# Performance work log

Measured on AMD Instinct MI355X. Metric: run time of the kernel, lower is better.

## Reference

```python
import jax, jax.numpy as jnp
import numpy as np

N, T, F_IN, F_OUT, E = 20000, 4, 64, 64, 640000


def setup_inputs() -> dict:
    key = jax.random.key(0)
    k1, k2, k3, k4, k5, k6 = jax.random.split(key, 6)
    node_features = jax.random.normal(k1, (N, T, F_IN), dtype=jnp.float32)
    edge_weights = jax.random.uniform(k2, (T, E), dtype=jnp.float32)
    src = jax.random.randint(k3, (E,), 0, N, dtype=jnp.int32)
    dst = jax.random.randint(k4, (E,), 0, N, dtype=jnp.int32)
    W = jax.random.normal(k5, (F_OUT, F_IN), dtype=jnp.float32) / np.sqrt(F_IN)
    b = jax.random.normal(k6, (F_OUT,), dtype=jnp.float32) * 0.01
    return {"node_features": node_features, "edge_weights": edge_weights,
            "src": src, "dst": dst, "W": W, "b": b}


def reference(node_features, edge_weights, src, dst, W, b):
    # u_mul_e: gather source node features and scale by per-edge, per-time weight
    # edge_weights (T, E) -> transposed (E, T) -> broadcast over feature dim
    msg = node_features[src] * edge_weights.T[:, :, None]          # (E, T, F_IN)
    # fn.sum: scatter-sum messages into destination nodes
    h = jax.ops.segment_sum(msg, dst, num_segments=node_features.shape[0])  # (N, T, F_IN)
    # nn.Linear(in_features, out_features)
    return h @ W.T + b                                             # (N, T, F_OUT)
```

## Files before the change

### kernel.cpp

```cpp
#include <hip/hip_runtime.h>

#define N_NODES 20000
#define T_STEPS 4
#define F_DIM   64
#define E_EDGES 640000
#define ROWS    (N_NODES * T_STEPS)
#define ROW_ELEMS (T_STEPS * F_DIM)

#define SCATTER_BLOCKS   (E_EDGES / 1024)
#define TRANSFORM_BLOCKS (ROWS / 64)
#define OVF_CAP          4096

__device__ __forceinline__ unsigned short f32_to_bf16_rne(float f) {
    unsigned u = __float_as_uint(f);
    u += 0x7FFFu + ((u >> 16) & 1u);
    return (unsigned short)(u >> 16);
}
__device__ __forceinline__ float bf16_to_f32(unsigned short h) {
    return __uint_as_float((unsigned)h << 16);
}

__global__ __launch_bounds__(256) void fused_build_kernel(
    const float* __restrict__ x, const float* __restrict__ W,
    unsigned short* __restrict__ yb,
    const int* __restrict__ src, const int* __restrict__ dst,
    const float* __restrict__ ew,
    int* __restrict__ cnt, int4* __restrict__ buckets, int cap,
    int4* __restrict__ ovf, int* __restrict__ ovf_cnt)
{
    if (blockIdx.x < SCATTER_BLOCKS) {
        const int base = blockIdx.x * 1024 + threadIdx.x;
#pragma unroll
        for (int j = 0; j < 4; ++j) {
            const int e = base + j * 256;
            const int d = dst[e];
            int4 rec;
            rec.x = src[e];
            rec.y = (unsigned)f32_to_bf16_rne(ew[e]) |
                    ((unsigned)f32_to_bf16_rne(ew[E_EDGES + e]) << 16);
            rec.z = (unsigned)f32_to_bf16_rne(ew[2 * E_EDGES + e]) |
                    ((unsigned)f32_to_bf16_rne(ew[3 * E_EDGES + e]) << 16);
            rec.w = d;
            const int pos = atomicAdd(&cnt[d], 1);
            if (pos < cap) {
                buckets[(size_t)d * cap + pos] = rec;
            } else {
                const int o = atomicAdd(ovf_cnt, 1);
                if (o < OVF_CAP) ovf[o] = rec;
            }
        }
        return;
    }

    __shared__ float xs[64 * 68];
    __shared__ float wt[64 * 68];
    const int tid  = threadIdx.x;
    const int row0 = (blockIdx.x - SCATTER_BLOCKS) * 64;

    {
        const int o  = tid & 63;
        const int fb = (tid >> 6) * 16;
#pragma unroll
        for (int k = 0; k < 16; ++k) {
            const int f = fb + k;
            wt[f * 68 + o] = W[o * 64 + f];
        }
    }
    {
        const float4* xg = (const float4*)(x + (size_t)row0 * 64);
#pragma unroll
        for (int k = 0; k < 4; ++k) {
            const int q  = k * 256 + tid;
            const int r  = q >> 4;
            const int c4 = (q & 15) * 4;
            *(float4*)&xs[r * 68 + c4] = xg[q];
        }
    }
    __syncthreads();

    const int rg = tid >> 4;
    const int oq = (tid & 15) * 4;

    float acc[4][4];
#pragma unroll
    for (int i = 0; i < 4; ++i)
#pragma unroll
        for (int j = 0; j < 4; ++j) acc[i][j] = 0.0f;

    for (int f = 0; f < 64; ++f) {
        const float4 w4 = *(const float4*)&wt[f * 68 + oq];
#pragma unroll
        for (int i = 0; i < 4; ++i) {
            const float xv = xs[(rg * 4 + i) * 68 + f];
            acc[i][0] += xv * w4.x;
            acc[i][1] += xv * w4.y;
            acc[i][2] += xv * w4.z;
            acc[i][3] += xv * w4.w;
        }
    }

#pragma unroll
    for (int i = 0; i < 4; ++i) {
        const int r = row0 + rg * 4 + i;
        ushort4 h;
        h.x = f32_to_bf16_rne(acc[i][0]);
        h.y = f32_to_bf16_rne(acc[i][1]);
        h.z = f32_to_bf16_rne(acc[i][2]);
        h.w = f32_to_bf16_rne(acc[i][3]);
        *(ushort4*)(yb + (size_t)r * 64 + oq) = h;
    }
}

__global__ __launch_bounds__(256) void accumulate_kernel(
    const unsigned short* __restrict__ yb, const int* __restrict__ cnt,
    const int4* __restrict__ buckets, int cap,
    const float* __restrict__ b, float* __restrict__ out)
{
    const int lane = threadIdx.x & 63;
    const int n    = blockIdx.x * 4 + (threadIdx.x >> 6);
    const int t    = lane >> 4;
    const int l4   = lane * 4;

    int deg = cnt[n];
    if (deg > cap) deg = cap;
    const int4* rp = buckets + (size_t)n * cap;

    float4 acc = make_float4(0.f, 0.f, 0.f, 0.f);

    int k = 0;
    for (; k + 8 <= deg; k += 8) {
        int4 r[8];
#pragma unroll
        for (int i = 0; i < 8; ++i) r[i] = rp[k + i];
        ushort4 v[8];
#pragma unroll
        for (int i = 0; i < 8; ++i)
            v[i] = *(const ushort4*)(yb + (size_t)r[i].x * ROW_ELEMS + l4);
#pragma unroll
        for (int i = 0; i < 8; ++i) {
            const unsigned word = (t & 2) ? (unsigned)r[i].z : (unsigned)r[i].y;
            const float w = bf16_to_f32((t & 1) ? (unsigned short)(word >> 16)
                                                : (unsigned short)(word & 0xFFFF));
            acc.x += bf16_to_f32(v[i].x) * w;
            acc.y += bf16_to_f32(v[i].y) * w;
            acc.z += bf16_to_f32(v[i].z) * w;
            acc.w += bf16_to_f32(v[i].w) * w;
        }
    }
    if (k + 4 <= deg) {
        int4 r[4];
#pragma unroll
        for (int i = 0; i < 4; ++i) r[i] = rp[k + i];
        ushort4 v[4];
#pragma unroll
        for (int i = 0; i < 4; ++i)
            v[i] = *(const ushort4*)(yb + (size_t)r[i].x * ROW_ELEMS + l4);
#pragma unroll
        for (int i = 0; i < 4; ++i) {
            const unsigned word = (t & 2) ? (unsigned)r[i].z : (unsigned)r[i].y;
            const float w = bf16_to_f32((t & 1) ? (unsigned short)(word >> 16)
                                                : (unsigned short)(word & 0xFFFF));
            acc.x += bf16_to_f32(v[i].x) * w;
            acc.y += bf16_to_f32(v[i].y) * w;
            acc.z += bf16_to_f32(v[i].z) * w;
            acc.w += bf16_to_f32(v[i].w) * w;
        }
        k += 4;
    }
    for (; k < deg; ++k) {
        const int4 r = rp[k];
        const unsigned word = (t & 2) ? (unsigned)r.z : (unsigned)r.y;
        const float w = bf16_to_f32((t & 1) ? (unsigned short)(word >> 16)
                                            : (unsigned short)(word & 0xFFFF));
        const ushort4 v = *(const ushort4*)(yb + (size_t)r.x * ROW_ELEMS + l4);
        acc.x += bf16_to_f32(v.x) * w;
        acc.y += bf16_to_f32(v.y) * w;
        acc.z += bf16_to_f32(v.z) * w;
        acc.w += bf16_to_f32(v.w) * w;
    }

    const float4 bv = *(const float4*)(b + (lane & 15) * 4);
    acc.x += bv.x; acc.y += bv.y; acc.z += bv.z; acc.w += bv.w;
    *(float4*)(out + (size_t)n * ROW_ELEMS + l4) = acc;
}

__global__ __launch_bounds__(256) void overflow_kernel(
    const unsigned short* __restrict__ yb, const int4* __restrict__ ovf,
    const int* __restrict__ ovf_cnt, float* __restrict__ out)
{
    const int lane = threadIdx.x & 63;
    const int w_id = threadIdx.x >> 6;
    const int t    = lane >> 4;
    const int l4   = lane * 4;
    int m = *ovf_cnt;
    if (m > OVF_CAP) m = OVF_CAP;
    for (int i = w_id; i < m; i += 4) {
        const int4 r = ovf[i];
        const unsigned word = (t & 2) ? (unsigned)r.z : (unsigned)r.y;
        const float w = bf16_to_f32((t & 1) ? (unsigned short)(word >> 16)
                                            : (unsigned short)(word & 0xFFFF));
        const ushort4 v = *(const ushort4*)(yb + (size_t)r.x * ROW_ELEMS + l4);
        float* op = out + (size_t)r.w * ROW_ELEMS + l4;
        atomicAdd(op + 0, bf16_to_f32(v.x) * w);
        atomicAdd(op + 1, bf16_to_f32(v.y) * w);
        atomicAdd(op + 2, bf16_to_f32(v.z) * w);
        atomicAdd(op + 3, bf16_to_f32(v.w) * w);
    }
}

extern "C" void kernel_launch(void* const* d_in, const int* in_sizes, int n_in,
                              void* d_out, int out_size, void* d_ws, size_t ws_size,
                              hipStream_t stream) {
    const float* x   = (const float*)d_in[0];
    const float* ew  = (const float*)d_in[1];
    const int*   src = (const int*)  d_in[2];
    const int*   dst = (const int*)  d_in[3];
    const float* W   = (const float*)d_in[4];
    const float* b   = (const float*)d_in[5];
    float*       out = (float*)d_out;

    char* ws = (char*)d_ws;
    size_t off = 0;
    auto alloc = [&](size_t bytes) {
        void* p = ws + off;
        off += (bytes + 255) & ~(size_t)255;
        return p;
    };
    unsigned short* yb  = (unsigned short*)alloc((size_t)ROWS * 64 * 2);
    int*            cnt = (int*) alloc((N_NODES + 1) * sizeof(int));
    int4*           ovf = (int4*)alloc((size_t)OVF_CAP * sizeof(int4));
    int*            ovf_cnt = cnt + N_NODES;

    size_t rem = (ws_size > off) ? (ws_size - off) : 0;
    int cap = (int)(rem / ((size_t)N_NODES * sizeof(int4)));
    if (cap > 128) cap = 128;
    if (cap < 1) cap = 1;
    int4* buckets = (int4*)(ws + off);

    hipMemsetAsync(cnt, 0, (N_NODES + 1) * sizeof(int), stream);
    fused_build_kernel<<<SCATTER_BLOCKS + TRANSFORM_BLOCKS, 256, 0, stream>>>(
        x, W, yb, src, dst, ew, cnt, buckets, cap, ovf, ovf_cnt);
    accumulate_kernel<<<N_NODES / 4, 256, 0, stream>>>(
        yb, cnt, buckets, cap, b, out);
    overflow_kernel<<<1, 256, 0, stream>>>(yb, ovf, ovf_cnt, out);
}
```

Measured before the change: 169.6 us.

## Use time-major transformed features and split accumulation per time step across blocks

The transformed feature buffer is now stored time-major, so each time slice of 20000x64 bf16 values is contiguous. The accumulate kernel launches one block per (node group, time step); each wave handles four edges at once in lane groups and reduces with shuffles. Scatter and transform blocks are interleaved 2:1 in the fused launch, and each scatter block now handles 256 edges. The aim is to shrink the working set per gather so it stays in cache and to raise parallelism. The cost is reading each edge record four times and a cross-lane reduction step.

Result: slower. 175.4 us (+3.5%).

```diff
diff --git a/kernel.cpp b/kernel.cpp
--- a/kernel.cpp
+++ b/kernel.cpp
@@ -7,8 +7,9 @@
 #define ROWS    (N_NODES * T_STEPS)
 #define ROW_ELEMS (T_STEPS * F_DIM)
 
-#define SCATTER_BLOCKS   (E_EDGES / 1024)
+#define SCATTER_BLOCKS   2500
 #define TRANSFORM_BLOCKS (ROWS / 64)
+#define FUSED_BLOCKS     (SCATTER_BLOCKS + TRANSFORM_BLOCKS)
 #define OVF_CAP          4096
 
 __device__ __forceinline__ unsigned short f32_to_bf16_rne(float f) {
@@ -18,6 +19,11 @@
 }
 __device__ __forceinline__ float bf16_to_f32(unsigned short h) {
     return __uint_as_float((unsigned)h << 16);
+}
+__device__ __forceinline__ float rec_weight(const int4& r, int t) {
+    const unsigned word = (t & 2) ? (unsigned)r.z : (unsigned)r.y;
+    return bf16_to_f32((t & 1) ? (unsigned short)(word >> 16)
+                               : (unsigned short)(word & 0xFFFF));
 }
 
 __global__ __launch_bounds__(256) void fused_build_kernel(
@@ -28,26 +34,24 @@
     int* __restrict__ cnt, int4* __restrict__ buckets, int cap,
     int4* __restrict__ ovf, int* __restrict__ ovf_cnt)
 {
-    if (blockIdx.x < SCATTER_BLOCKS) {
-        const int base = blockIdx.x * 1024 + threadIdx.x;
-#pragma unroll
-        for (int j = 0; j < 4; ++j) {
-            const int e = base + j * 256;
-            const int d = dst[e];
-            int4 rec;
-            rec.x = src[e];
-            rec.y = (unsigned)f32_to_bf16_rne(ew[e]) |
-                    ((unsigned)f32_to_bf16_rne(ew[E_EDGES + e]) << 16);
-            rec.z = (unsigned)f32_to_bf16_rne(ew[2 * E_EDGES + e]) |
-                    ((unsigned)f32_to_bf16_rne(ew[3 * E_EDGES + e]) << 16);
-            rec.w = d;
-            const int pos = atomicAdd(&cnt[d], 1);
-            if (pos < cap) {
-                buckets[(size_t)d * cap + pos] = rec;
-            } else {
-                const int o = atomicAdd(ovf_cnt, 1);
-                if (o < OVF_CAP) ovf[o] = rec;
-            }
+    const int m = blockIdx.x % 3;
+    if (m != 2) {
+        const int sidx = (blockIdx.x / 3) * 2 + m;
+        const int e    = sidx * 256 + threadIdx.x;
+        const int d = dst[e];
+        int4 rec;
+        rec.x = src[e];
+        rec.y = (unsigned)f32_to_bf16_rne(ew[e]) |
+                ((unsigned)f32_to_bf16_rne(ew[E_EDGES + e]) << 16);
+        rec.z = (unsigned)f32_to_bf16_rne(ew[2 * E_EDGES + e]) |
+                ((unsigned)f32_to_bf16_rne(ew[3 * E_EDGES + e]) << 16);
+        rec.w = d;
+        const int pos = atomicAdd(&cnt[d], 1);
+        if (pos < cap) {
+            buckets[(size_t)d * cap + pos] = rec;
+        } else {
+            const int o = atomicAdd(ovf_cnt, 1);
+            if (o < OVF_CAP) ovf[o] = rec;
         }
         return;
     }
@@ -55,7 +59,7 @@
     __shared__ float xs[64 * 68];
     __shared__ float wt[64 * 68];
     const int tid  = threadIdx.x;
-    const int row0 = (blockIdx.x - SCATTER_BLOCKS) * 64;
+    const int row0 = (blockIdx.x / 3) * 64;
 
     {
         const int o  = tid & 63;
@@ -99,15 +103,15 @@
         }
     }
 
+    const int node = (row0 >> 2) + rg;
 #pragma unroll
     for (int i = 0; i < 4; ++i) {
-        const int r = row0 + rg * 4 + i;
         ushort4 h;
         h.x = f32_to_bf16_rne(acc[i][0]);
         h.y = f32_to_bf16_rne(acc[i][1]);
         h.z = f32_to_bf16_rne(acc[i][2]);
         h.w = f32_to_bf16_rne(acc[i][3]);
-        *(ushort4*)(yb + (size_t)r * 64 + oq) = h;
+        *(ushort4*)(yb + ((size_t)i * N_NODES + node) * 64 + oq) = h;
     }
 }
 
@@ -117,71 +121,57 @@
     const float* __restrict__ b, float* __restrict__ out)
 {
     const int lane = threadIdx.x & 63;
-    const int n    = blockIdx.x * 4 + (threadIdx.x >> 6);
-    const int t    = lane >> 4;
-    const int l4   = lane * 4;
+    const int wv   = threadIdx.x >> 6;
+    const int t    = blockIdx.x & 3;
+    const int n    = (blockIdx.x >> 2) * 4 + wv;
+    const int g    = lane >> 4;
+    const int f4   = (lane & 15) * 4;
 
     int deg = cnt[n];
     if (deg > cap) deg = cap;
     const int4* rp = buckets + (size_t)n * cap;
+    const unsigned short* yt = yb + (size_t)t * N_NODES * 64;
 
     float4 acc = make_float4(0.f, 0.f, 0.f, 0.f);
 
     int k = 0;
     for (; k + 8 <= deg; k += 8) {
-        int4 r[8];
-#pragma unroll
-        for (int i = 0; i < 8; ++i) r[i] = rp[k + i];
-        ushort4 v[8];
-#pragma unroll
-        for (int i = 0; i < 8; ++i)
-            v[i] = *(const ushort4*)(yb + (size_t)r[i].x * ROW_ELEMS + l4);
-#pragma unroll
-        for (int i = 0; i < 8; ++i) {
-            const unsigned word = (t & 2) ? (unsigned)r[i].z : (unsigned)r[i].y;
-            const float w = bf16_to_f32((t & 1) ? (unsigned short)(word >> 16)
-                                                : (unsigned short)(word & 0xFFFF));
-            acc.x += bf16_to_f32(v[i].x) * w;
-            acc.y += bf16_to_f32(v[i].y) * w;
-            acc.z += bf16_to_f32(v[i].z) * w;
-            acc.w += bf16_to_f32(v[i].w) * w;
-        }
-    }
-    if (k + 4 <= deg) {
-        int4 r[4];
-#pragma unroll
-        for (int i = 0; i < 4; ++i) r[i] = rp[k + i];
-        ushort4 v[4];
-#pragma unroll
-        for (int i = 0; i < 4; ++i)
-            v[i] = *(const ushort4*)(yb + (size_t)r[i].x * ROW_ELEMS + l4);
-#pragma unroll
-        for (int i = 0; i < 4; ++i) {
-            const unsigned word = (t & 2) ? (unsigned)r[i].z : (unsigned)r[i].y;
-            const float w = bf16_to_f32((t & 1) ? (unsigned short)(word >> 16)
-                                                : (unsigned short)(word & 0xFFFF));
-            acc.x += bf16_to_f32(v[i].x) * w;
-            acc.y += bf16_to_f32(v[i].y) * w;
-            acc.z += bf16_to_f32(v[i].z) * w;
-            acc.w += bf16_to_f32(v[i].w) * w;
-        }
-        k += 4;
-    }
-    for (; k < deg; ++k) {
-        const int4 r = rp[k];
-        const unsigned word = (t & 2) ? (unsigned)r.z : (unsigned)r.y;
-        const float w = bf16_to_f32((t & 1) ? (unsigned short)(word >> 16)
-                                            : (unsigned short)(word & 0xFFFF));
-        const ushort4 v = *(const ushort4*)(yb + (size_t)r.x * ROW_ELEMS + l4);
-        acc.x += bf16_to_f32(v.x) * w;
-        acc.y += bf16_to_f32(v.y) * w;
-        acc.z += bf16_to_f32(v.z) * w;
-        acc.w += bf16_to_f32(v.w) * w;
-    }
-
-    const float4 bv = *(const float4*)(b + (lane & 15) * 4);
-    acc.x += bv.x; acc.y += bv.y; acc.z += bv.z; acc.w += bv.w;
-    *(float4*)(out + (size_t)n * ROW_ELEMS + l4) = acc;
+        const int4 r0 = rp[k + g];
+        const int4 r1 = rp[k + 4 + g];
+        const ushort4 v0 = *(const ushort4*)(yt + (size_t)r0.x * 64 + f4);
+        const ushort4 v1 = *(const ushort4*)(yt + (size_t)r1.x * 64 + f4);
+        const float w0 = rec_weight(r0, t);
+        const float w1 = rec_weight(r1, t);
+        acc.x += bf16_to_f32(v0.x) * w0 + bf16_to_f32(v1.x) * w1;
+        acc.y += bf16_to_f32(v0.y) * w0 + bf16_to_f32(v1.y) * w1;
+        acc.z += bf16_to_f32(v0.z) * w0 + bf16_to_f32(v1.z) * w1;
+        acc.w += bf16_to_f32(v0.w) * w0 + bf16_to_f32(v1.w) * w1;
+    }
+    if (k < deg) {
+        const int i0 = k + g;
+        const int i1 = k + 4 + g;
+        const int4 r0 = rp[(i0 < deg) ? i0 : k];
+        const int4 r1 = rp[(i1 < deg) ? i1 : k];
+        const float w0 = (i0 < deg) ? rec_weight(r0, t) : 0.f;
+        const float w1 = (i1 < deg) ? rec_weight(r1, t) : 0.f;
+        const ushort4 v0 = *(const ushort4*)(yt + (size_t)r0.x * 64 + f4);
+        const ushort4 v1 = *(const ushort4*)(yt + (size_t)r1.x * 64 + f4);
+        acc.x += bf16_to_f32(v0.x) * w0 + bf16_to_f32(v1.x) * w1;
+        acc.y += bf16_to_f32(v0.y) * w0 + bf16_to_f32(v1.y) * w1;
+        acc.z += bf16_to_f32(v0.z) * w0 + bf16_to_f32(v1.z) * w1;
+        acc.w += bf16_to_f32(v0.w) * w0 + bf16_to_f32(v1.w) * w1;
+    }
+
+    acc.x += __shfl_xor(acc.x, 16); acc.y += __shfl_xor(acc.y, 16);
+    acc.z += __shfl_xor(acc.z, 16); acc.w += __shfl_xor(acc.w, 16);
+    acc.x += __shfl_xor(acc.x, 32); acc.y += __shfl_xor(acc.y, 32);
+    acc.z += __shfl_xor(acc.z, 32); acc.w += __shfl_xor(acc.w, 32);
+
+    if (g == 0) {
+        const float4 bv = *(const float4*)(b + f4);
+        acc.x += bv.x; acc.y += bv.y; acc.z += bv.z; acc.w += bv.w;
+        *(float4*)(out + (size_t)n * ROW_ELEMS + t * F_DIM + f4) = acc;
+    }
 }
 
 __global__ __launch_bounds__(256) void overflow_kernel(
@@ -191,16 +181,15 @@
     const int lane = threadIdx.x & 63;
     const int w_id = threadIdx.x >> 6;
     const int t    = lane >> 4;
-    const int l4   = lane * 4;
+    const int f4   = (lane & 15) * 4;
     int m = *ovf_cnt;
     if (m > OVF_CAP) m = OVF_CAP;
     for (int i = w_id; i < m; i += 4) {
         const int4 r = ovf[i];
-        const unsigned word = (t & 2) ? (unsigned)r.z : (unsigned)r.y;
-        const float w = bf16_to_f32((t & 1) ? (unsigned short)(word >> 16)
-                                            : (unsigned short)(word & 0xFFFF));
-        const ushort4 v = *(const ushort4*)(yb + (size_t)r.x * ROW_ELEMS + l4);
-        float* op = out + (size_t)r.w * ROW_ELEMS + l4;
+        const float w = rec_weight(r, t);
+        const ushort4 v = *(const ushort4*)(
+            yb + ((size_t)t * N_NODES + r.x) * 64 + f4);
+        float* op = out + (size_t)r.w * ROW_ELEMS + lane * 4;
         atomicAdd(op + 0, bf16_to_f32(v.x) * w);
         atomicAdd(op + 1, bf16_to_f32(v.y) * w);
         atomicAdd(op + 2, bf16_to_f32(v.z) * w);
@@ -238,9 +227,9 @@
     int4* buckets = (int4*)(ws + off);
 
     hipMemsetAsync(cnt, 0, (N_NODES + 1) * sizeof(int), stream);
-    fused_build_kernel<<<SCATTER_BLOCKS + TRANSFORM_BLOCKS, 256, 0, stream>>>(
+    fused_build_kernel<<<FUSED_BLOCKS, 256, 0, stream>>>(
         x, W, yb, src, dst, ew, cnt, buckets, cap, ovf, ovf_cnt);
-    accumulate_kernel<<<N_NODES / 4, 256, 0, stream>>>(
+    accumulate_kernel<<<(N_NODES / 4) * T_STEPS, 256, 0, stream>>>(
         yb, cnt, buckets, cap, b, out);
     overflow_kernel<<<1, 256, 0, stream>>>(yb, ovf, ovf_cnt, out);
 }
```

## Interleave scatter and transform blocks, fold overflow into accumulate, deepen unroll

Applied to the files above, without the earlier changes.

Reorganizes the fused build grid so scatter blocks (now 256 edges each) and GEMM transform blocks interleave 2:1, letting atomic-bound scatter work overlap compute-bound transform work across CUs. Bucket records are written with nontemporal stores to avoid polluting cache. The accumulate loop is unrolled to 16 records for more memory-level parallelism, and overflow edges are handled inside accumulate by a linear scan, removing the separate overflow launch and its float atomics. Deeper unroll raises register pressure, and the overflow scan is slow if many nodes overflow.

After: 176.0 us. 3.8% more time.

```diff
diff --git a/kernel.cpp b/kernel.cpp
--- a/kernel.cpp
+++ b/kernel.cpp
@@ -7,9 +7,12 @@
 #define ROWS    (N_NODES * T_STEPS)
 #define ROW_ELEMS (T_STEPS * F_DIM)
 
-#define SCATTER_BLOCKS   (E_EDGES / 1024)
+#define SCATTER_BLOCKS   2500
 #define TRANSFORM_BLOCKS (ROWS / 64)
+#define FUSED_BLOCKS     (SCATTER_BLOCKS + TRANSFORM_BLOCKS)
 #define OVF_CAP          4096
+
+typedef int   v4i  __attribute__((ext_vector_type(4)));
 
 __device__ __forceinline__ unsigned short f32_to_bf16_rne(float f) {
     unsigned u = __float_as_uint(f);
@@ -18,6 +21,11 @@
 }
 __device__ __forceinline__ float bf16_to_f32(unsigned short h) {
     return __uint_as_float((unsigned)h << 16);
+}
+__device__ __forceinline__ float rec_weight(const int4& r, int t) {
+    const unsigned word = (t & 2) ? (unsigned)r.z : (unsigned)r.y;
+    return bf16_to_f32((t & 1) ? (unsigned short)(word >> 16)
+                               : (unsigned short)(word & 0xFFFF));
 }
 
 __global__ __launch_bounds__(256) void fused_build_kernel(
@@ -28,26 +36,25 @@
     int* __restrict__ cnt, int4* __restrict__ buckets, int cap,
     int4* __restrict__ ovf, int* __restrict__ ovf_cnt)
 {
-    if (blockIdx.x < SCATTER_BLOCKS) {
-        const int base = blockIdx.x * 1024 + threadIdx.x;
-#pragma unroll
-        for (int j = 0; j < 4; ++j) {
-            const int e = base + j * 256;
-            const int d = dst[e];
-            int4 rec;
-            rec.x = src[e];
-            rec.y = (unsigned)f32_to_bf16_rne(ew[e]) |
-                    ((unsigned)f32_to_bf16_rne(ew[E_EDGES + e]) << 16);
-            rec.z = (unsigned)f32_to_bf16_rne(ew[2 * E_EDGES + e]) |
-                    ((unsigned)f32_to_bf16_rne(ew[3 * E_EDGES + e]) << 16);
-            rec.w = d;
-            const int pos = atomicAdd(&cnt[d], 1);
-            if (pos < cap) {
-                buckets[(size_t)d * cap + pos] = rec;
-            } else {
-                const int o = atomicAdd(ovf_cnt, 1);
-                if (o < OVF_CAP) ovf[o] = rec;
-            }
+    const int m = blockIdx.x % 3;
+    if (m != 2) {
+        const int sidx = (blockIdx.x / 3) * 2 + m;
+        const int e    = sidx * 256 + threadIdx.x;
+        const int d = dst[e];
+        int4 rec;
+        rec.x = src[e];
+        rec.y = (unsigned)f32_to_bf16_rne(ew[e]) |
+                ((unsigned)f32_to_bf16_rne(ew[E_EDGES + e]) << 16);
+        rec.z = (unsigned)f32_to_bf16_rne(ew[2 * E_EDGES + e]) |
+                ((unsigned)f32_to_bf16_rne(ew[3 * E_EDGES + e]) << 16);
+        rec.w = d;
+        const int pos = atomicAdd(&cnt[d], 1);
+        if (pos < cap) {
+            __builtin_nontemporal_store(*(const v4i*)&rec,
+                                        (v4i*)&buckets[(size_t)d * cap + pos]);
+        } else {
+            const int o = atomicAdd(ovf_cnt, 1);
+            if (o < OVF_CAP) ovf[o] = rec;
         }
         return;
     }
@@ -55,7 +62,7 @@
     __shared__ float xs[64 * 68];
     __shared__ float wt[64 * 68];
     const int tid  = threadIdx.x;
-    const int row0 = (blockIdx.x - SCATTER_BLOCKS) * 64;
+    const int row0 = (blockIdx.x / 3) * 64;
 
     {
         const int o  = tid & 63;
@@ -114,6 +121,7 @@
 __global__ __launch_bounds__(256) void accumulate_kernel(
     const unsigned short* __restrict__ yb, const int* __restrict__ cnt,
     const int4* __restrict__ buckets, int cap,
+    const int4* __restrict__ ovf, const int* __restrict__ ovf_cnt,
     const float* __restrict__ b, float* __restrict__ out)
 {
     const int lane = threadIdx.x & 63;
@@ -121,57 +129,69 @@
     const int t    = lane >> 4;
     const int l4   = lane * 4;
 
-    int deg = cnt[n];
-    if (deg > cap) deg = cap;
-    const int4* rp = buckets + (size_t)n * cap;
+    const int total = cnt[n];
+    const int deg   = (total > cap) ? cap : total;
+    const int4* rp  = buckets + (size_t)n * cap;
 
     float4 acc = make_float4(0.f, 0.f, 0.f, 0.f);
 
     int k = 0;
-    for (; k + 8 <= deg; k += 8) {
-        int4 r[8];
-#pragma unroll
-        for (int i = 0; i < 8; ++i) r[i] = rp[k + i];
-        ushort4 v[8];
-#pragma unroll
-        for (int i = 0; i < 8; ++i)
+    for (; k + 16 <= deg; k += 16) {
+        int4 r[16];
+#pragma unroll
+        for (int i = 0; i < 16; ++i) r[i] = rp[k + i];
+        ushort4 v[16];
+#pragma unroll
+        for (int i = 0; i < 16; ++i)
             v[i] = *(const ushort4*)(yb + (size_t)r[i].x * ROW_ELEMS + l4);
 #pragma unroll
-        for (int i = 0; i < 8; ++i) {
-            const unsigned word = (t & 2) ? (unsigned)r[i].z : (unsigned)r[i].y;
-            const float w = bf16_to_f32((t & 1) ? (unsigned short)(word >> 16)
-                                                : (unsigned short)(word & 0xFFFF));
+        for (int i = 0; i < 16; ++i) {
+            const float w = rec_weight(r[i], t);
             acc.x += bf16_to_f32(v[i].x) * w;
             acc.y += bf16_to_f32(v[i].y) * w;
             acc.z += bf16_to_f32(v[i].z) * w;
             acc.w += bf16_to_f32(v[i].w) * w;
         }
     }
-    if (k + 4 <= deg) {
-        int4 r[4];
-#pragma unroll
-        for (int i = 0; i < 4; ++i) r[i] = rp[k + i];
-        ushort4 v[4];
-#pragma unroll
-        for (int i = 0; i < 4; ++i)
+    if (k + 8 <= deg) {
+        int4 r[8];
+#pragma unroll
+        for (int i = 0; i < 8; ++i) r[i] = rp[k + i];
+        ushort4 v[8];
+#pragma unroll
+        for (int i = 0; i < 8; ++i)
             v[i] = *(const ushort4*)(yb + (size_t)r[i].x * ROW_ELEMS + l4);
 #pragma unroll
-        for (int i = 0; i < 4; ++i) {
-            const unsigned word = (t & 2) ? (unsigned)r[i].z : (unsigned)r[i].y;
-            const float w = bf16_to_f32((t & 1) ? (unsigned short)(word >> 16)
-                                                : (unsigned short)(word & 0xFFFF));
+        for (int i = 0; i < 8; ++i) {
+            const float w = rec_weight(r[i], t);
             acc.x += bf16_to_f32(v[i].x) * w;
             acc.y += bf16_to_f32(v[i].y) * w;
             acc.z += bf16_to_f32(v[i].z) * w;
             acc.w += bf16_to_f32(v[i].w) * w;
         }
+        k += 8;
+    }
+    if (k + 4 <= deg) {
+        int4 r[4];
+#pragma unroll
+        for (int i = 0; i < 4; ++i) r[i] = rp[k + i];
+        ushort4 v[4];
+#pragma unroll
+        for (int i = 0; i < 4; ++i)
+            v[i] = *(const ushort4*)(yb + (size_t)r[i].x * ROW_ELEMS + l4);
+#pragma unroll
+        for (int i = 0; i < 4; ++i) {
+            const float w = rec_weight(r[i], t);
+            acc.x += bf16_to_f32(v[i].x) * w;
+            acc.y += bf16_to_f32(v[i].y) * w;
+            acc.z += bf16_to_f32(v[i].z) * w;
+            acc.w += bf16_to_f32(v[i].w) * w;
+        }
         k += 4;
     }
     for (; k < deg; ++k) {
         const int4 r = rp[k];
-        const unsigned word = (t & 2) ? (unsigned)r.z : (unsigned)r.y;
-        const float w = bf16_to_f32((t & 1) ? (unsigned short)(word >> 16)
-                                            : (unsigned short)(word & 0xFFFF));
+        const float w = rec_weight(r, t);
         const ushort4 v = *(const ushort4*)(yb + (size_t)r.x * ROW_ELEMS + l4);
         acc.x += bf16_to_f32(v.x) * w;
         acc.y += bf16_to_f32(v.y) * w;
@@ -179,33 +199,24 @@
         acc.w += bf16_to_f32(v.w) * w;
     }
 
+    if (total > cap) {
+        int m = *ovf_cnt;
+        if (m > OVF_CAP) m = OVF_CAP;
+        for (int i = 0; i < m; ++i) {
+            const int4 r = ovf[i];
+            if (r.w != n) continue;
+            const float w = rec_weight(r, t);
+            const ushort4 v = *(const ushort4*)(yb + (size_t)r.x * ROW_ELEMS + l4);
+            acc.x += bf16_to_f32(v.x) * w;
+            acc.y += bf16_to_f32(v.y) * w;
+            acc.z += bf16_to_f32(v.z) * w;
+            acc.w += bf16_to_f32(v.w) * w;
+        }
+    }
+
     const float4 bv = *(const float4*)(b + (lane & 15) * 4);
     acc.x += bv.x; acc.y += bv.y; acc.z += bv.z; acc.w += bv.w;
     *(float4*)(out + (size_t)n * ROW_ELEMS + l4) = acc;
-}
-
-__global__ __launch_bounds__(256) void overflow_kernel(
-    const unsigned short* __restrict__ yb, const int4* __restrict__ ovf,
-    const int* __restrict__ ovf_cnt, float* __restrict__ out)
-{
-    const int lane = threadIdx.x & 63;
-    const int w_id = threadIdx.x >> 6;
-    const int t    = lane >> 4;
-    const int l4   = lane * 4;
-    int m = *ovf_cnt;
-    if (m > OVF_CAP) m = OVF_CAP;
-    for (int i = w_id; i < m; i += 4) {
-        const int4 r = ovf[i];
-        const unsigned word = (t & 2) ? (unsigned)r.z : (unsigned)r.y;
-        const float w = bf16_to_f32((t & 1) ? (unsigned short)(word >> 16)
-                                            : (unsigned short)(word & 0xFFFF));
-        const ushort4 v = *(const ushort4*)(yb + (size_t)r.x * ROW_ELEMS + l4);
-        float* op = out + (size_t)r.w * ROW_ELEMS + l4;
-        atomicAdd(op + 0, bf16_to_f32(v.x) * w);
-        atomicAdd(op + 1, bf16_to_f32(v.y) * w);
-        atomicAdd(op + 2, bf16_to_f32(v.z) * w);
-        atomicAdd(op + 3, bf16_to_f32(v.w) * w);
-    }
 }
 
 extern "C" void kernel_launch(void* const* d_in, const int* in_sizes, int n_in,
@@ -238,9 +249,8 @@
     int4* buckets = (int4*)(ws + off);
 
     hipMemsetAsync(cnt, 0, (N_NODES + 1) * sizeof(int), stream);
-    fused_build_kernel<<<SCATTER_BLOCKS + TRANSFORM_BLOCKS, 256, 0, stream>>>(
+    fused_build_kernel<<<FUSED_BLOCKS, 256, 0, stream>>>(
         x, W, yb, src, dst, ew, cnt, buckets, cap, ovf, ovf_cnt);
     accumulate_kernel<<<N_NODES / 4, 256, 0, stream>>>(
-        yb, cnt, buckets, cap, b, out);
-    overflow_kernel<<<1, 256, 0, stream>>>(yb, ovf, ovf_cnt, out);
-}
+        yb, cnt, buckets, cap, ovf, ovf_cnt, b, out);
+}
```
